# Kernel optimization log

Measured on AMD Instinct MI355X. Metric: run time of the kernel, lower is better.

## Reference

```python
import jax, jax.numpy as jnp
import numpy as np

B = 2
N_FINE = 100000
N_COARSE = 25000
H = 128
IN_DIM = 2 * H + 1  # 257


def setup_inputs() -> dict:
    key = jax.random.key(0)
    ks = jax.random.split(key, 10)
    s_in = 1.0 / np.sqrt(IN_DIM)
    s_h = 1.0 / np.sqrt(H)
    return {
        "x": jax.random.normal(ks[0], (B, N_COARSE, H), dtype=jnp.float32),
        "x_scale": jax.random.normal(ks[1], (B, N_FINE, H), dtype=jnp.float32),
        "fine2coarse_index": jax.random.randint(ks[2], (N_FINE,), 0, N_COARSE),
        "distances": jax.random.uniform(ks[3], (1, N_FINE, 1), dtype=jnp.float32),
        "W1": jax.random.uniform(ks[4], (IN_DIM, H), minval=-s_in, maxval=s_in, dtype=jnp.float32),
        "b1": jax.random.uniform(ks[5], (H,), minval=-s_in, maxval=s_in, dtype=jnp.float32),
        "W2": jax.random.uniform(ks[6], (H, H), minval=-s_h, maxval=s_h, dtype=jnp.float32),
        "b2": jax.random.uniform(ks[7], (H,), minval=-s_h, maxval=s_h, dtype=jnp.float32),
        "W3": jax.random.uniform(ks[8], (H, H), minval=-s_h, maxval=s_h, dtype=jnp.float32),
        "b3": jax.random.uniform(ks[9], (H,), minval=-s_h, maxval=s_h, dtype=jnp.float32),
    }


def reference(x, x_scale, fine2coarse_index, distances, W1, b1, W2, b2, W3, b3):
    # gather coarse features to fine nodes: [B, N_fine, H]
    xg = jnp.take(x, fine2coarse_index, axis=1)
    d = jnp.broadcast_to(distances, (xg.shape[0], xg.shape[1], 1))
    h = jnp.concatenate([xg, x_scale, d], axis=2)  # [B, N_fine, 2H+1]
    # MLP: Linear -> SiLU -> Linear -> SiLU -> Linear
    h = jax.nn.silu(h @ W1 + b1)
    h = jax.nn.silu(h @ W2 + b2)
    return h @ W3 + b3
```

## Files before the change

### kernel.cpp

```cpp
#include <hip/hip_runtime.h>
#include <math.h>

#define H 128
#define NF 100000
#define NC 25000
#define TM 64

typedef _Float16 f16;
typedef f16 f16x8 __attribute__((ext_vector_type(8)));
typedef f16 f16x4 __attribute__((ext_vector_type(4)));
typedef float f32x4 __attribute__((ext_vector_type(4)));

#define MFMA16(a, b, c) __builtin_amdgcn_mfma_f32_16x16x32_f16((a), (b), (c), 0, 0, 0)


__global__ void prep_w(const float* __restrict__ W1, const float* __restrict__ W2,
                       const float* __restrict__ W3, f16* __restrict__ ws)
{
    int i = blockIdx.x * 256 + threadIdx.x;
    if (i < 32768) {
        int j = i & 7, lane = (i >> 3) & 63, kk = (i >> 9) & 7, nt = i >> 12;
        int n = nt * 16 + (lane & 15);
        int k = kk * 32 + (lane >> 4) * 8 + j;
        ws[i] = (f16)W1[k * H + n];
    } else if (i < 49152) {
        int q = i - 32768;
        int j = q & 7, lane = (q >> 3) & 63, kk = (q >> 9) & 3, nt = q >> 11;
        int n = nt * 16 + (lane & 15);
        int k = kk * 32 + (lane >> 4) * 8 + j;
        ws[i] = (f16)W2[k * H + n];
    } else {
        int q = i - 49152;
        int j = q & 7, lane = (q >> 3) & 63, kk = (q >> 9) & 3, nt = q >> 11;
        int n = nt * 16 + (lane & 15);
        int k = kk * 32 + (lane >> 4) * 8 + j;
        ws[i] = (f16)W3[k * H + n];
    }
}

__device__ __forceinline__ float silu_f(float v) {
    return v / (1.0f + __expf(-v));
}

__global__
void fused_mlp_v18(const float* __restrict__ x,
                   const float* __restrict__ xsc,
                   const int*   __restrict__ f2c,
                   const float* __restrict__ dist,
                   const float* __restrict__ W1,
                   const float* __restrict__ b1,
                   const float* __restrict__ b2,
                   const float* __restrict__ b3,
                   const f16*   __restrict__ ws,
                   float* __restrict__ out)
{
    __shared__ __align__(16) f16 sA[TM * H];
    __shared__ float sD[TM];
    __shared__ int   sCI[TM];

    const int t = threadIdx.x;
    const int l = t & 63, w = t >> 6;
    const int wRow = (w >> 1) * 32;
    const int wnt  = (w & 1) * 4;
    const int lr = l & 15, lg = l >> 4;
    const int R0 = blockIdx.x * TM;

    if (t < TM) {
        int Rs = R0 + t;
        int bb = Rs >= NF;
        int nn = Rs - bb * NF;
        sCI[t] = bb * NC + f2c[nn];
        sD[t]  = dist[nn];
    }
    __syncthreads();

    const f16* F1 = ws;
    const f16* F2 = ws + 32768;
    const f16* F3 = ws + 49152;

    f32x4 acc[2][4];
    #pragma unroll
    for (int nt = 0; nt < 4; ++nt) {
        int col = (wnt + nt) * 16 + lr;
        float bc = b1[col];
        float wc = W1[256 * H + col];
        #pragma unroll
        for (int mt = 0; mt < 2; ++mt)
            #pragma unroll
            for (int r = 0; r < 4; ++r)
                acc[mt][nt][r] = bc + sD[wRow + mt * 16 + lg * 4 + r] * wc;
    }

    #pragma unroll
    for (int i = 0; i < 8; ++i) {
        int f = i * 256 + t;
        int row = f >> 5, col = (f & 31) * 4;
        float4 v = *(const float4*)(x + (long long)sCI[row] * H + col);
        f16x4 hv; hv[0] = (f16)v.x; hv[1] = (f16)v.y; hv[2] = (f16)v.z; hv[3] = (f16)v.w;
        *(f16x4*)(sA + row * H + (((col >> 3) ^ (row & 7)) << 3) + (col & 7)) = hv;
    }
    __syncthreads();

    #pragma unroll
    for (int kk = 0; kk < 4; ++kk) {
        f16x8 wv[4];
        #pragma unroll
        for (int nt = 0; nt < 4; ++nt)
            wv[nt] = *(const f16x8*)(F1 + ((((wnt + nt) * 8 + kk) * 64 + l) << 3));
        int k = kk * 32 + (lg << 3);
        int slot = (((k >> 3) ^ (lr & 7)) << 3);
        f16x8 a0 = *(const f16x8*)(sA + (wRow + lr) * H + slot);
        f16x8 a1 = *(const f16x8*)(sA + (wRow + 16 + lr) * H + slot);
        #pragma unroll
        for (int nt = 0; nt < 4; ++nt) {
            acc[0][nt] = MFMA16(a0, wv[nt], acc[0][nt]);
            acc[1][nt] = MFMA16(a1, wv[nt], acc[1][nt]);
        }
    }
    __syncthreads();

    #pragma unroll
    for (int i = 0; i < 8; ++i) {
        int f = i * 256 + t;
        int row = f >> 5, col = (f & 31) * 4;
        float4 v = *(const float4*)(xsc + (long long)(R0 + row) * H + col);
        f16x4 hv; hv[0] = (f16)v.x; hv[1] = (f16)v.y; hv[2] = (f16)v.z; hv[3] = (f16)v.w;
        *(f16x4*)(sA + row * H + (((col >> 3) ^ (row & 7)) << 3) + (col & 7)) = hv;
    }
    __syncthreads();

    #pragma unroll
    for (int kk = 0; kk < 4; ++kk) {
        f16x8 wv[4];
        #pragma unroll
        for (int nt = 0; nt < 4; ++nt)
            wv[nt] = *(const f16x8*)(F1 + ((((wnt + nt) * 8 + kk + 4) * 64 + l) << 3));
        int k = kk * 32 + (lg << 3);
        int slot = (((k >> 3) ^ (lr & 7)) << 3);
        f16x8 a0 = *(const f16x8*)(sA + (wRow + lr) * H + slot);
        f16x8 a1 = *(const f16x8*)(sA + (wRow + 16 + lr) * H + slot);
        #pragma unroll
        for (int nt = 0; nt < 4; ++nt) {
            acc[0][nt] = MFMA16(a0, wv[nt], acc[0][nt]);
            acc[1][nt] = MFMA16(a1, wv[nt], acc[1][nt]);
        }
    }
    __syncthreads();

    #pragma unroll
    for (int nt = 0; nt < 4; ++nt)
        #pragma unroll
        for (int mt = 0; mt < 2; ++mt)
            #pragma unroll
            for (int r = 0; r < 4; ++r) {
                int row = wRow + mt * 16 + lg * 4 + r;
                int col = (wnt + nt) * 16 + lr;
                sA[row * H + (((col >> 3) ^ (row & 7)) << 3) + (col & 7)] =
                    (f16)silu_f(acc[mt][nt][r]);
            }
    __syncthreads();

    #pragma unroll
    for (int nt = 0; nt < 4; ++nt) {
        float bc = b2[(wnt + nt) * 16 + lr];
        #pragma unroll
        for (int mt = 0; mt < 2; ++mt)
            #pragma unroll
            for (int r = 0; r < 4; ++r)
                acc[mt][nt][r] = bc;
    }
    #pragma unroll
    for (int kk = 0; kk < 4; ++kk) {
        f16x8 wv[4];
        #pragma unroll
        for (int nt = 0; nt < 4; ++nt)
            wv[nt] = *(const f16x8*)(F2 + ((((wnt + nt) * 4 + kk) * 64 + l) << 3));
        int k = kk * 32 + (lg << 3);
        int slot = (((k >> 3) ^ (lr & 7)) << 3);
        f16x8 a0 = *(const f16x8*)(sA + (wRow + lr) * H + slot);
        f16x8 a1 = *(const f16x8*)(sA + (wRow + 16 + lr) * H + slot);
        #pragma unroll
        for (int nt = 0; nt < 4; ++nt) {
            acc[0][nt] = MFMA16(a0, wv[nt], acc[0][nt]);
            acc[1][nt] = MFMA16(a1, wv[nt], acc[1][nt]);
        }
    }
    __syncthreads();

    #pragma unroll
    for (int nt = 0; nt < 4; ++nt)
        #pragma unroll
        for (int mt = 0; mt < 2; ++mt)
            #pragma unroll
            for (int r = 0; r < 4; ++r) {
                int row = wRow + mt * 16 + lg * 4 + r;
                int col = (wnt + nt) * 16 + lr;
                sA[row * H + (((col >> 3) ^ (row & 7)) << 3) + (col & 7)] =
                    (f16)silu_f(acc[mt][nt][r]);
            }
    __syncthreads();

    #pragma unroll
    for (int nt = 0; nt < 4; ++nt) {
        float bc = b3[(wnt + nt) * 16 + lr];
        #pragma unroll
        for (int mt = 0; mt < 2; ++mt)
            #pragma unroll
            for (int r = 0; r < 4; ++r)
                acc[mt][nt][r] = bc;
    }
    #pragma unroll
    for (int kk = 0; kk < 4; ++kk) {
        f16x8 wv[4];
        #pragma unroll
        for (int nt = 0; nt < 4; ++nt)
            wv[nt] = *(const f16x8*)(F3 + ((((wnt + nt) * 4 + kk) * 64 + l) << 3));
        int k = kk * 32 + (lg << 3);
        int slot = (((k >> 3) ^ (lr & 7)) << 3);
        f16x8 a0 = *(const f16x8*)(sA + (wRow + lr) * H + slot);
        f16x8 a1 = *(const f16x8*)(sA + (wRow + 16 + lr) * H + slot);
        #pragma unroll
        for (int nt = 0; nt < 4; ++nt) {
            acc[0][nt] = MFMA16(a0, wv[nt], acc[0][nt]);
            acc[1][nt] = MFMA16(a1, wv[nt], acc[1][nt]);
        }
    }

    #pragma unroll
    for (int mt = 0; mt < 2; ++mt)
        #pragma unroll
        for (int nt = 0; nt < 4; ++nt)
            #pragma unroll
            for (int r = 0; r < 4; ++r) {
                long long row = (long long)R0 + wRow + mt * 16 + lg * 4 + r;
                int col = (wnt + nt) * 16 + lr;
                out[row * H + col] = acc[mt][nt][r];
            }
}

extern "C" void kernel_launch(void* const* d_in, const int* in_sizes, int n_in,
                              void* d_out, int out_size, void* d_ws, size_t ws_size,
                              hipStream_t stream)
{
    const float* x    = (const float*)d_in[0];
    const float* xsc  = (const float*)d_in[1];
    const int*   f2c  = (const int*)d_in[2];
    const float* dist = (const float*)d_in[3];
    const float* W1   = (const float*)d_in[4];
    const float* b1   = (const float*)d_in[5];
    const float* W2   = (const float*)d_in[6];
    const float* b2   = (const float*)d_in[7];
    const float* W3   = (const float*)d_in[8];
    const float* b3   = (const float*)d_in[9];
    f16* ws = (f16*)d_ws;

    prep_w<<<256, 256, 0, stream>>>(W1, W2, W3, ws);

    const int n_rows = 2 * NF;
    dim3 grid(n_rows / TM);
    fused_mlp_v18<<<grid, 256, 0, stream>>>(x, xsc, f2c, dist, W1, b1, b2, b3,
                                            ws, (float*)d_out);
}
```

Measured before the change: 77.06 us.

## Double-buffer shared memory and prefetch x_scale before the gather

```diff
diff --git a/kernel.cpp b/kernel.cpp
--- a/kernel.cpp
+++ b/kernel.cpp
@@ -43,7 +43,7 @@
 }
 
 __global__
-void fused_mlp_v18(const float* __restrict__ x,
+void fused_mlp_v19(const float* __restrict__ x,
                    const float* __restrict__ xsc,
                    const int*   __restrict__ f2c,
                    const float* __restrict__ dist,
@@ -54,7 +54,8 @@
                    const f16*   __restrict__ ws,
                    float* __restrict__ out)
 {
-    __shared__ __align__(16) f16 sA[TM * H];
+    __shared__ __align__(16) f16 sG[TM * H];
+    __shared__ __align__(16) f16 sS[TM * H];
     __shared__ float sD[TM];
     __shared__ int   sCI[TM];
 
@@ -65,6 +66,16 @@
     const int lr = l & 15, lg = l >> 4;
     const int R0 = blockIdx.x * TM;
 
+    f16x4 vxs[8];
+    #pragma unroll
+    for (int i = 0; i < 8; ++i) {
+        int f = i * 256 + t;
+        int row = f >> 5, col = (f & 31) * 4;
+        float4 v = *(const float4*)(xsc + (long long)(R0 + row) * H + col);
+        f16x4 hv; hv[0] = (f16)v.x; hv[1] = (f16)v.y; hv[2] = (f16)v.z; hv[3] = (f16)v.w;
+        vxs[i] = hv;
+    }
+
     if (t < TM) {
         int Rs = R0 + t;
         int bb = Rs >= NF;
@@ -97,38 +108,32 @@
         int row = f >> 5, col = (f & 31) * 4;
         float4 v = *(const float4*)(x + (long long)sCI[row] * H + col);
         f16x4 hv; hv[0] = (f16)v.x; hv[1] = (f16)v.y; hv[2] = (f16)v.z; hv[3] = (f16)v.w;
-        *(f16x4*)(sA + row * H + (((col >> 3) ^ (row & 7)) << 3) + (col & 7)) = hv;
-    }
-    __syncthreads();
-
-    #pragma unroll
-    for (int kk = 0; kk < 4; ++kk) {
-        f16x8 wv[4];
-        #pragma unroll
-        for (int nt = 0; nt < 4; ++nt)
-            wv[nt] = *(const f16x8*)(F1 + ((((wnt + nt) * 8 + kk) * 64 + l) << 3));
-        int k = kk * 32 + (lg << 3);
-        int slot = (((k >> 3) ^ (lr & 7)) << 3);
-        f16x8 a0 = *(const f16x8*)(sA + (wRow + lr) * H + slot);
-        f16x8 a1 = *(const f16x8*)(sA + (wRow + 16 + lr) * H + slot);
-        #pragma unroll
-        for (int nt = 0; nt < 4; ++nt) {
-            acc[0][nt] = MFMA16(a0, wv[nt], acc[0][nt]);
-            acc[1][nt] = MFMA16(a1, wv[nt], acc[1][nt]);
-        }
-    }
-    __syncthreads();
-
+        *(f16x4*)(sG + row * H + (((col >> 3) ^ (row & 7)) << 3) + (col & 7)) = hv;
+    }
     #pragma unroll
     for (int i = 0; i < 8; ++i) {
         int f = i * 256 + t;
         int row = f >> 5, col = (f & 31) * 4;
-        float4 v = *(const float4*)(xsc + (long long)(R0 + row) * H + col);
-        f16x4 hv; hv[0] = (f16)v.x; hv[1] = (f16)v.y; hv[2] = (f16)v.z; hv[3] = (f16)v.w;
-        *(f16x4*)(sA + row * H + (((col >> 3) ^ (row & 7)) << 3) + (col & 7)) = hv;
-    }
-    __syncthreads();
-
+        *(f16x4*)(sS + row * H + (((col >> 3) ^ (row & 7)) << 3) + (col & 7)) = vxs[i];
+    }
+    __syncthreads();
+
+    #pragma unroll
+    for (int kk = 0; kk < 4; ++kk) {
+        f16x8 wv[4];
+        #pragma unroll
+        for (int nt = 0; nt < 4; ++nt)
+            wv[nt] = *(const f16x8*)(F1 + ((((wnt + nt) * 8 + kk) * 64 + l) << 3));
+        int k = kk * 32 + (lg << 3);
+        int slot = (((k >> 3) ^ (lr & 7)) << 3);
+        f16x8 a0 = *(const f16x8*)(sG + (wRow + lr) * H + slot);
+        f16x8 a1 = *(const f16x8*)(sG + (wRow + 16 + lr) * H + slot);
+        #pragma unroll
+        for (int nt = 0; nt < 4; ++nt) {
+            acc[0][nt] = MFMA16(a0, wv[nt], acc[0][nt]);
+            acc[1][nt] = MFMA16(a1, wv[nt], acc[1][nt]);
+        }
+    }
     #pragma unroll
     for (int kk = 0; kk < 4; ++kk) {
         f16x8 wv[4];
@@ -137,8 +142,8 @@
             wv[nt] = *(const f16x8*)(F1 + ((((wnt + nt) * 8 + kk + 4) * 64 + l) << 3));
         int k = kk * 32 + (lg << 3);
         int slot = (((k >> 3) ^ (lr & 7)) << 3);
-        f16x8 a0 = *(const f16x8*)(sA + (wRow + lr) * H + slot);
-        f16x8 a1 = *(const f16x8*)(sA + (wRow + 16 + lr) * H + slot);
+        f16x8 a0 = *(const f16x8*)(sS + (wRow + lr) * H + slot);
+        f16x8 a1 = *(const f16x8*)(sS + (wRow + 16 + lr) * H + slot);
         #pragma unroll
         for (int nt = 0; nt < 4; ++nt) {
             acc[0][nt] = MFMA16(a0, wv[nt], acc[0][nt]);
@@ -155,7 +160,7 @@
             for (int r = 0; r < 4; ++r) {
                 int row = wRow + mt * 16 + lg * 4 + r;
                 int col = (wnt + nt) * 16 + lr;
-                sA[row * H + (((col >> 3) ^ (row & 7)) << 3) + (col & 7)] =
+                sG[row * H + (((col >> 3) ^ (row & 7)) << 3) + (col & 7)] =
                     (f16)silu_f(acc[mt][nt][r]);
             }
     __syncthreads();
@@ -177,15 +182,14 @@
             wv[nt] = *(const f16x8*)(F2 + ((((wnt + nt) * 4 + kk) * 64 + l) << 3));
         int k = kk * 32 + (lg << 3);
         int slot = (((k >> 3) ^ (lr & 7)) << 3);
-        f16x8 a0 = *(const f16x8*)(sA + (wRow + lr) * H + slot);
-        f16x8 a1 = *(const f16x8*)(sA + (wRow + 16 + lr) * H + slot);
-        #pragma unroll
-        for (int nt = 0; nt < 4; ++nt) {
-            acc[0][nt] = MFMA16(a0, wv[nt], acc[0][nt]);
-            acc[1][nt] = MFMA16(a1, wv[nt], acc[1][nt]);
-        }
-    }
-    __syncthreads();
+        f16x8 a0 = *(const f16x8*)(sG + (wRow + lr) * H + slot);
+        f16x8 a1 = *(const f16x8*)(sG + (wRow + 16 + lr) * H + slot);
+        #pragma unroll
+        for (int nt = 0; nt < 4; ++nt) {
+            acc[0][nt] = MFMA16(a0, wv[nt], acc[0][nt]);
+            acc[1][nt] = MFMA16(a1, wv[nt], acc[1][nt]);
+        }
+    }
 
     #pragma unroll
     for (int nt = 0; nt < 4; ++nt)
@@ -195,7 +199,7 @@
             for (int r = 0; r < 4; ++r) {
                 int row = wRow + mt * 16 + lg * 4 + r;
                 int col = (wnt + nt) * 16 + lr;
-                sA[row * H + (((col >> 3) ^ (row & 7)) << 3) + (col & 7)] =
+                sS[row * H + (((col >> 3) ^ (row & 7)) << 3) + (col & 7)] =
                     (f16)silu_f(acc[mt][nt][r]);
             }
     __syncthreads();
@@ -217,8 +221,8 @@
             wv[nt] = *(const f16x8*)(F3 + ((((wnt + nt) * 4 + kk) * 64 + l) << 3));
         int k = kk * 32 + (lg << 3);
         int slot = (((k >> 3) ^ (lr & 7)) << 3);
-        f16x8 a0 = *(const f16x8*)(sA + (wRow + lr) * H + slot);
-        f16x8 a1 = *(const f16x8*)(sA + (wRow + 16 + lr) * H + slot);
+        f16x8 a0 = *(const f16x8*)(sS + (wRow + lr) * H + slot);
+        f16x8 a1 = *(const f16x8*)(sS + (wRow + 16 + lr) * H + slot);
         #pragma unroll
         for (int nt = 0; nt < 4; ++nt) {
             acc[0][nt] = MFMA16(a0, wv[nt], acc[0][nt]);
@@ -258,6 +262,6 @@
 
     const int n_rows = 2 * NF;
     dim3 grid(n_rows / TM);
-    fused_mlp_v18<<<grid, 256, 0, stream>>>(x, xsc, f2c, dist, W1, b1, b2, b3,
+    fused_mlp_v19<<<grid, 256, 0, stream>>>(x, xsc, f2c, dist, W1, b1, b2, b3,
                                             ws, (float*)d_out);
 }
```

New measurement: 85.67 us. 1.11x slower.
